# Optimization experiments

Hardware: AMD Instinct MI355X
Metric: run time of the kernel (lower is better)

## Reference

```python
import jax, jax.numpy as jnp
import numpy as np

B, C, H, N = 4, 128, 4, 2048
D = C // H  # head_dim = 32
BN_EPS = 1e-5


def _conv1(w, b, x):
    # 1x1 Conv1d: [O,C] x [B,C,N] -> [B,O,N]
    return jnp.einsum('oc,bcn->bon', w, x) + b[None, :, None]


def setup_inputs() -> dict:
    key = jax.random.key(0)
    ks = jax.random.split(key, 20)
    p = lambda k, shape: jax.random.normal(k, shape, dtype=jnp.float32) * 0.05
    return {
        'x1': jax.random.normal(ks[0], (B, C, N), dtype=jnp.float32),
        'x2': jax.random.normal(ks[1], (B, C, N), dtype=jnp.float32),
        'kv_mask': jnp.ones((B, N), dtype=bool),
        'wq': p(ks[2], (C, C)), 'bq': p(ks[3], (C,)),
        'wk': p(ks[4], (C, C)), 'bk': p(ks[5], (C,)),
        'wv': p(ks[6], (C, C)), 'bv': p(ks[7], (C,)),
        'wm': p(ks[8], (C, C)), 'bm': p(ks[9], (C,)),
        'wc1': p(ks[10], (2 * C, 2 * C)), 'bc1': p(ks[11], (2 * C,)),
        'bn_gamma': jnp.ones((2 * C,), dtype=jnp.float32),
        'bn_beta': jnp.zeros((2 * C,), dtype=jnp.float32),
        'bn_mean': p(ks[12], (2 * C,)),
        'bn_var': jax.random.uniform(ks[13], (2 * C,), dtype=jnp.float32, minval=0.5, maxval=1.5),
        'wc2': p(ks[14], (C, 2 * C)), 'bc2': p(ks[15], (C,)),
    }


def reference(x1, x2, kv_mask, wq, bq, wk, bk, wv, bv, wm, bm,
              wc1, bc1, bn_gamma, bn_beta, bn_mean, bn_var, wc2, bc2):
    b, _, n = x1.shape
    q = _conv1(wq, bq, x1).reshape(b, H, D, n)   # bhdn
    k = _conv1(wk, bk, x2).reshape(b, H, D, -1)  # bhdm
    v = _conv1(wv, bv, x2).reshape(b, H, D, -1)  # bhdm
    qk = jnp.einsum('bhdn,bhdm->bhnm', q, k)
    # masked_fill on raw QK before scaling, matching torch code
    qk = jnp.where(kv_mask[:, None, None, :], qk, jnp.float32(-1e6))
    score = jax.nn.softmax(qk * (1.0 / D ** 0.5), axis=-1)
    add_value = jnp.einsum('bhnm,bhdm->bhdn', score, v).reshape(b, C, n)
    add_value = _conv1(wm, bm, add_value)
    cat = jnp.concatenate([x1, add_value], axis=1)  # [B, 2C, N]
    h = _conv1(wc1, bc1, cat)
    # BatchNorm1d in inference mode (running stats)
    h = (h - bn_mean[None, :, None]) * jax.lax.rsqrt(bn_var[None, :, None] + BN_EPS)
    h = h * bn_gamma[None, :, None] + bn_beta[None, :, None]
    h = jax.nn.relu(h)
    h = _conv1(wc2, bc2, h)
    return x1 + h
```

## Files before the change

### kernel.cpp

```cpp
#include <hip/hip_runtime.h>

typedef __attribute__((ext_vector_type(4))) float v4f;
typedef __attribute__((ext_vector_type(8))) _Float16 half8;
typedef __attribute__((ext_vector_type(4))) _Float16 half4;
typedef __attribute__((ext_vector_type(2))) _Float16 half2t;

constexpr float C2 = 0.17677669529663687f * 1.44269504088896341f;

__device__ __forceinline__ half4 pk4(float a, float b, float c, float d) {
  half2t lo = __builtin_bit_cast(half2t, __builtin_amdgcn_cvt_pkrtz(a, b));
  half2t hi = __builtin_bit_cast(half2t, __builtin_amdgcn_cvt_pkrtz(c, d));
  return __builtin_shufflevector(lo, hi, 0, 1, 2, 3);
}

__global__ __launch_bounds__(512) void prep(
    const float* __restrict__ wq, const float* __restrict__ wk,
    const float* __restrict__ wv, const float* __restrict__ wm,
    const float* __restrict__ wc1, const float* __restrict__ wc2,
    const unsigned char* __restrict__ mask, _Float16* __restrict__ wqkvh,
    _Float16* __restrict__ wts, float* __restrict__ maskf) {
  const int e = (blockIdx.x * 512 + threadIdx.x) * 4;
  if (e < 49152) {
    const float* src;
    int base;
    if (e < 16384) { src = wq; base = 0; }
    else if (e < 32768) { src = wk; base = 16384; }
    else { src = wv; base = 32768; }
    const float4 t = *(const float4*)(src + (e - base));
    *(half4*)(wqkvh + e) = pk4(t.x, t.y, t.z, t.w);
  } else if (e < 196608) {
    const int e2 = e - 49152;
    const float* src;
    int base, cols;
    if (e2 < 16384) { src = wm; base = 0; cols = 128; }
    else if (e2 < 81920) { src = wc1; base = 16384; cols = 256; }
    else { src = wc2; base = 81920; cols = 256; }
    const int le = e2 - base;
    const int r = le / cols, c = le % cols;
    const int kt = c >> 4, q4 = (c >> 2) & 3;
    const int dst = r * cols + ((kt >> 1) << 5) + (q4 << 3) + ((kt & 1) << 2);
    const float4 t = *(const float4*)(src + le);
    *(half4*)(wts + base + dst) = pk4(t.x, t.y, t.z, t.w);
  } else {
    const int e2 = e - 196608;
    const unsigned mv = *(const unsigned*)(mask + e2);
    float4 o;
    o.x = (mv & 0x000000ffu) ? 0.f : -1.0e6f * C2;
    o.y = (mv & 0x0000ff00u) ? 0.f : -1.0e6f * C2;
    o.z = (mv & 0x00ff0000u) ? 0.f : -1.0e6f * C2;
    o.w = (mv & 0xff000000u) ? 0.f : -1.0e6f * C2;
    *(float4*)(maskf + e2) = o;
  }
}

__global__ __launch_bounds__(512, 4) void qkv(
    const float* __restrict__ x1, const float* __restrict__ x2,
    const _Float16* __restrict__ wqkvh, const float* __restrict__ bq,
    const float* __restrict__ bk, const float* __restrict__ bv,
    _Float16* __restrict__ Qpk, _Float16* __restrict__ Kpk,
    _Float16* __restrict__ Vpk) {
  const int b = blockIdx.y;
  const int bx = blockIdx.x;
  const int tid = threadIdx.x, w = tid >> 6, lane = tid & 63;
  const int l = lane & 15, q = lane >> 4;
  const int n0 = bx * 32;
  const _Float16* wqh = wqkvh;
  const _Float16* wkh = wqkvh + 16384;
  const _Float16* wvh = wqkvh + 32768;

  __shared__ _Float16 x1s[2][16 * 136];
  __shared__ _Float16 x2s[2][16 * 136];

  {
    const int ch = tid >> 2, seg = tid & 3;
#pragma unroll
    for (int g = 0; g < 2; ++g) {
      const float4 a =
          *(const float4*)(x1 + (size_t)(b * 128 + ch) * 2048 + n0 + g * 16 + seg * 4);
      const float4 c =
          *(const float4*)(x2 + (size_t)(b * 128 + ch) * 2048 + n0 + g * 16 + seg * 4);
      x1s[g][(seg * 4 + 0) * 136 + ch] = (_Float16)a.x;
      x1s[g][(seg * 4 + 1) * 136 + ch] = (_Float16)a.y;
      x1s[g][(seg * 4 + 2) * 136 + ch] = (_Float16)a.z;
      x1s[g][(seg * 4 + 3) * 136 + ch] = (_Float16)a.w;
      x2s[g][(seg * 4 + 0) * 136 + ch] = (_Float16)c.x;
      x2s[g][(seg * 4 + 1) * 136 + ch] = (_Float16)c.y;
      x2s[g][(seg * 4 + 2) * 136 + ch] = (_Float16)c.z;
      x2s[g][(seg * 4 + 3) * 136 + ch] = (_Float16)c.w;
    }
  }
  __syncthreads();

#pragma unroll
  for (int i = 0; i < 3; ++i) {
    const int t = w * 3 + i;
    if (t < 8) {
      const int mt = t;
      half8 wf[4];
#pragma unroll
      for (int kt = 0; kt < 4; ++kt)
        wf[kt] = *(const half8*)(wqh + (mt * 16 + l) * 128 + kt * 32 + q * 8);
      const v4f bias = *(const v4f*)(bq + mt * 16 + q * 4);
#pragma unroll
      for (int g = 0; g < 2; ++g) {
        v4f acc = bias;
#pragma unroll
        for (int kt = 0; kt < 4; ++kt) {
          const half8 xf = *(const half8*)&x1s[g][l * 136 + kt * 32 + q * 8];
          acc = __builtin_amdgcn_mfma_f32_16x16x32_f16(wf[kt], xf, acc, 0, 0, 0);
        }
        *(half4*)(Qpk + ((size_t)(b * 8 + mt) * 2048 + n0 + g * 16 + l) * 16 + q * 4) =
            pk4(acc[0] * C2, acc[1] * C2, acc[2] * C2, acc[3] * C2);
      }
    } else if (t < 16) {
      const int mt = t - 8;
      half8 wf[4];
#pragma unroll
      for (int kt = 0; kt < 4; ++kt)
        wf[kt] = *(const half8*)(wkh + (mt * 16 + l) * 128 + kt * 32 + q * 8);
      const v4f bias = *(const v4f*)(bk + mt * 16 + q * 4);
#pragma unroll
      for (int g = 0; g < 2; ++g) {
        v4f acc = bias;
#pragma unroll
        for (int kt = 0; kt < 4; ++kt) {
          const half8 xf = *(const half8*)&x2s[g][l * 136 + kt * 32 + q * 8];
          acc = __builtin_amdgcn_mfma_f32_16x16x32_f16(wf[kt], xf, acc, 0, 0, 0);
        }
        *(half4*)(Kpk + ((size_t)(b * 8 + mt) * 2048 + n0 + g * 16 + l) * 16 + q * 4) =
            pk4(acc[0], acc[1], acc[2], acc[3]);
      }
    } else {
      const int ot = t - 16;
      half8 wf[4];
#pragma unroll
      for (int kt = 0; kt < 4; ++kt)
        wf[kt] = *(const half8*)(wvh + (ot * 16 + l) * 128 + kt * 32 + q * 8);
      const float bvv = bv[ot * 16 + l];
#pragma unroll
      for (int g = 0; g < 2; ++g) {
        v4f acc = {bvv, bvv, bvv, bvv};
#pragma unroll
        for (int kt = 0; kt < 4; ++kt) {
          const half8 xf = *(const half8*)&x2s[g][l * 136 + kt * 32 + q * 8];
          acc = __builtin_amdgcn_mfma_f32_16x16x32_f16(xf, wf[kt], acc, 0, 0, 0);
        }
        const int kx = bx * 2 + g;
        *(half4*)(Vpk + (((size_t)(b * 4 + (ot >> 1)) * 128 + kx) * 32 +
                         (ot & 1) * 16 + l) * 16 + q * 4) =
            pk4(acc[0], acc[1], acc[2], acc[3]);
      }
    }
  }
}

__global__ __launch_bounds__(256) void attn(
    const _Float16* __restrict__ Qpk, const _Float16* __restrict__ Kpk,
    const _Float16* __restrict__ Vpk, const float* __restrict__ maskf,
    _Float16* __restrict__ Opk, float* __restrict__ lsump) {
  const int bh = blockIdx.y, b = bh >> 2, h = bh & 3;
  const int part = blockIdx.z;
  const int tid = threadIdx.x, w = tid >> 6, lane = tid & 63;
  const int l = lane & 15, q = lane >> 4;
  const int nb = blockIdx.x * 128 + w * 32;

  __shared__ _Float16 ldsK[2][3088];
  __shared__ _Float16 ldsV[2][3072];
  __shared__ __align__(16) float biass[512];

  const size_t qrow = (size_t)(b * 8 + h * 2 + (q >> 1)) * 2048;
  const half8 qf0 = *(const half8*)(Qpk + (qrow + nb + l) * 16 + (q & 1) * 8);
  const half8 qf1 = *(const half8*)(Qpk + (qrow + nb + 16 + l) * 16 + (q & 1) * 8);
  const _Float16* __restrict__ Kg = Kpk + (size_t)(b * 8 + h * 2) * 2048 * 16;
  const _Float16* __restrict__ Vg = Vpk + (size_t)((b * 4 + h) * 128) * 512;

  const int kct = tid >> 7, kk = (tid >> 1) & 63, khf = tid & 1;
  const int vt = tid >> 6, vd = (tid >> 1) & 31;

  v4f oacc[2][2] = {{{0.f, 0.f, 0.f, 0.f}, {0.f, 0.f, 0.f, 0.f}},
                    {{0.f, 0.f, 0.f, 0.f}, {0.f, 0.f, 0.f, 0.f}}};
  float ls0 = 0.f, ls1 = 0.f;
  const int mbeg = part * 512;

  if (tid < 128)
    *(float4*)&biass[tid * 4] = *(const float4*)(maskf + b * 2048 + mbeg + tid * 4);
  half8 kr = *(const half8*)(Kg + ((size_t)kct * 2048 + mbeg + kk) * 16 + khf * 8);
  half8 vr = *(const half8*)(Vg + (size_t)((mbeg >> 4) + vt) * 512 + vd * 16 + khf * 8);
  *(half8*)&ldsK[0][kct * 1544 + kk * 24 + khf * 8] = kr;
  *(half8*)&ldsV[0][vt * 768 + vd * 24 + khf * 8] = vr;
  __syncthreads();

  for (int i = 0; i < 8; ++i) {
    const int m0 = mbeg + i * 64;
    const int cur = i & 1;
    if (i < 7) {
      kr = *(const half8*)(Kg + ((size_t)kct * 2048 + m0 + 64 + kk) * 16 + khf * 8);
      vr = *(const half8*)(Vg + (size_t)(((m0 + 64) >> 4) + vt) * 512 + vd * 16 + khf * 8);
    }
    half4 pB[2][4];
#pragma unroll
    for (int mt = 0; mt < 4; ++mt) {
      const half8 kf =
          *(const half8*)&ldsK[cur][(q >> 1) * 1544 + (mt * 16 + l) * 24 + (q & 1) * 8];
      const v4f biasv = *(const v4f*)&biass[i * 64 + mt * 16 + q * 4];
      __builtin_amdgcn_s_setprio(1);
      const v4f s0 = __builtin_amdgcn_mfma_f32_16x16x32_f16(kf, qf0, biasv, 0, 0, 0);
      const v4f s1 = __builtin_amdgcn_mfma_f32_16x16x32_f16(kf, qf1, biasv, 0, 0, 0);
      __builtin_amdgcn_s_setprio(0);
      const float a0 = exp2f(s0[0]), a1 = exp2f(s0[1]), a2 = exp2f(s0[2]),
                  a3 = exp2f(s0[3]);
      const float c0 = exp2f(s1[0]), c1 = exp2f(s1[1]), c2 = exp2f(s1[2]),
                  c3 = exp2f(s1[3]);
      ls0 += (a0 + a1) + (a2 + a3);
      ls1 += (c0 + c1) + (c2 + c3);
      pB[0][mt] = pk4(a0, a1, a2, a3);
      pB[1][mt] = pk4(c0, c1, c2, c3);
    }
    __builtin_amdgcn_s_setprio(1);
#pragma unroll
    for (int mt = 0; mt < 4; ++mt) {
      const half4 vf0 = *(const half4*)&ldsV[cur][mt * 768 + l * 24 + q * 4];
      const half4 vf1 = *(const half4*)&ldsV[cur][mt * 768 + (16 + l) * 24 + q * 4];
      oacc[0][0] = __builtin_amdgcn_mfma_f32_16x16x16f16(vf0, pB[0][mt], oacc[0][0], 0, 0, 0);
      oacc[0][1] = __builtin_amdgcn_mfma_f32_16x16x16f16(vf1, pB[0][mt], oacc[0][1], 0, 0, 0);
      oacc[1][0] = __builtin_amdgcn_mfma_f32_16x16x16f16(vf0, pB[1][mt], oacc[1][0], 0, 0, 0);
      oacc[1][1] = __builtin_amdgcn_mfma_f32_16x16x16f16(vf1, pB[1][mt], oacc[1][1], 0, 0, 0);
    }
    __builtin_amdgcn_s_setprio(0);
    if (i < 7) {
      *(half8*)&ldsK[cur ^ 1][kct * 1544 + kk * 24 + khf * 8] = kr;
      *(half8*)&ldsV[cur ^ 1][vt * 768 + vd * 24 + khf * 8] = vr;
      __syncthreads();
    }
  }
  ls0 += __shfl_xor(ls0, 16);
  ls0 += __shfl_xor(ls0, 32);
  ls1 += __shfl_xor(ls1, 16);
  ls1 += __shfl_xor(ls1, 32);
  if (q == 0) {
    lsump[part * 32768 + bh * 2048 + nb + l] = ls0;
    lsump[part * 32768 + bh * 2048 + nb + 16 + l] = ls1;
  }
#pragma unroll
  for (int qt = 0; qt < 2; ++qt)
#pragma unroll
    for (int df = 0; df < 2; ++df)
      *(half4*)(Opk + (size_t)part * 1048576 +
                ((size_t)(b * 8 + h * 2 + df) * 2048 + nb + qt * 16 + l) * 16 +
                q * 4) = pk4(oacc[qt][df][0], oacc[qt][df][1], oacc[qt][df][2],
                             oacc[qt][df][3]);
}

__global__ __launch_bounds__(512, 4) void post(
    const float* __restrict__ x1, const _Float16* __restrict__ Opk,
    const float* __restrict__ lsump, const _Float16* __restrict__ wts,
    const float* __restrict__ bm, const float* __restrict__ bc1,
    const float* __restrict__ gamma, const float* __restrict__ beta,
    const float* __restrict__ mean, const float* __restrict__ var,
    const float* __restrict__ bc2, float* __restrict__ out) {
  const int b = blockIdx.y;
  const int n0 = blockIdx.x * 32;
  const int tid = threadIdx.x, w = tid >> 6, lane = tid & 63;
  const int l = lane & 15, q = lane >> 4;
  const _Float16* wm_h = wts;
  const _Float16* wc1_h = wts + 16384;
  const _Float16* wc2_h = wts + 81920;

  __shared__ __align__(16) float x1s[2][16 * 132];
  __shared__ __align__(16) _Float16 ofs[2][8 * 256];
  __shared__ __align__(16) _Float16 catl[2][16 * 256];
  __shared__ __align__(16) _Float16 exB[2][16 * 256];

  {
    const int ch = tid >> 2, seg = tid & 3;
#pragma unroll
    for (int g = 0; g < 2; ++g) {
      const float4 a =
          *(const float4*)(x1 + (size_t)(b * 128 + ch) * 2048 + n0 + g * 16 + seg * 4);
      x1s[g][(seg * 4 + 0) * 132 + ch] = a.x;
      x1s[g][(seg * 4 + 1) * 132 + ch] = a.y;
      x1s[g][(seg * 4 + 2) * 132 + ch] = a.z;
      x1s[g][(seg * 4 + 3) * 132 + ch] = a.w;
    }
  }
  {
#pragma unroll
    for (int g = 0; g < 2; ++g) {
      const int n = n0 + g * 16 + l;
      const size_t idx = (size_t)(b * 4 + (w >> 1)) * 2048 + n;
      const float rl = 1.0f / (lsump[idx] + lsump[32768 + idx] +
                               lsump[65536 + idx] + lsump[98304 + idx]);
      const size_t oa = ((size_t)(b * 8 + w) * 2048 + n) * 16 + q * 4;
      const half4 a = *(const half4*)(Opk + oa);
      const half4 c = *(const half4*)(Opk + 1048576 + oa);
      const half4 d = *(const half4*)(Opk + 2097152 + oa);
      const half4 e = *(const half4*)(Opk + 3145728 + oa);
      const _Float16 rh = (_Float16)rl;
      const half4 rl4 = {rh, rh, rh, rh};
      *(half4*)&ofs[g][w * 256 + l * 16 + q * 4] = ((a + c) + (d + e)) * rl4;
    }
  }
  __syncthreads();
  {
#pragma unroll
    for (int g = 0; g < 2; ++g) {
      const float4 xv = *(const float4*)&x1s[g][l * 132 + w * 16 + q * 4];
      *(half4*)&catl[g][w * 256 + l * 16 + q * 4] = pk4(xv.x, xv.y, xv.z, xv.w);
    }
  }
  {
    const v4f bias = *(const v4f*)(bm + w * 16 + q * 4);
    v4f acc[2] = {bias, bias};
#pragma unroll
    for (int kt2 = 0; kt2 < 4; ++kt2) {
      const half8 wp = *(const half8*)(wm_h + (w * 16 + l) * 128 + kt2 * 32 + q * 8);
      const half4 wlo = __builtin_shufflevector(wp, wp, 0, 1, 2, 3);
      const half4 whi = __builtin_shufflevector(wp, wp, 4, 5, 6, 7);
#pragma unroll
      for (int g = 0; g < 2; ++g) {
        const half4 of0 = *(const half4*)&ofs[g][(kt2 * 2) * 256 + l * 16 + q * 4];
        const half4 of1 = *(const half4*)&ofs[g][(kt2 * 2 + 1) * 256 + l * 16 + q * 4];
        acc[g] = __builtin_amdgcn_mfma_f32_16x16x16f16(wlo, of0, acc[g], 0, 0, 0);
        acc[g] = __builtin_amdgcn_mfma_f32_16x16x16f16(whi, of1, acc[g], 0, 0, 0);
      }
    }
#pragma unroll
    for (int g = 0; g < 2; ++g)
      *(half4*)&catl[g][(8 + w) * 256 + l * 16 + q * 4] =
          pk4(acc[g][0], acc[g][1], acc[g][2], acc[g][3]);
  }
  __syncthreads();
#pragma unroll
  for (int i = 0; i < 2; ++i) {
    const int mt = w * 2 + i;
    const v4f bias = *(const v4f*)(bc1 + mt * 16 + q * 4);
    v4f acc[2] = {bias, bias};
#pragma unroll
    for (int kt2 = 0; kt2 < 8; ++kt2) {
      const half8 wp = *(const half8*)(wc1_h + (mt * 16 + l) * 256 + kt2 * 32 + q * 8);
      const half4 wlo = __builtin_shufflevector(wp, wp, 0, 1, 2, 3);
      const half4 whi = __builtin_shufflevector(wp, wp, 4, 5, 6, 7);
#pragma unroll
      for (int g = 0; g < 2; ++g) {
        const half4 f0 = *(const half4*)&catl[g][(kt2 * 2) * 256 + l * 16 + q * 4];
        const half4 f1 = *(const half4*)&catl[g][(kt2 * 2 + 1) * 256 + l * 16 + q * 4];
        acc[g] = __builtin_amdgcn_mfma_f32_16x16x16f16(wlo, f0, acc[g], 0, 0, 0);
        acc[g] = __builtin_amdgcn_mfma_f32_16x16x16f16(whi, f1, acc[g], 0, 0, 0);
      }
    }
    const v4f gm = *(const v4f*)(gamma + mt * 16 + q * 4);
    const v4f bt = *(const v4f*)(beta + mt * 16 + q * 4);
    const v4f mn = *(const v4f*)(mean + mt * 16 + q * 4);
    const v4f vr = *(const v4f*)(var + mt * 16 + q * 4);
#pragma unroll
    for (int g = 0; g < 2; ++g) {
      float hh[4];
#pragma unroll
      for (int r = 0; r < 4; ++r) {
        const float a1 = gm[r] * rsqrtf(vr[r] + 1e-5f);
        const float b1 = bt[r] - mn[r] * a1;
        hh[r] = fmaxf(acc[g][r] * a1 + b1, 0.f);
      }
      *(half4*)&exB[g][mt * 256 + l * 16 + q * 4] = pk4(hh[0], hh[1], hh[2], hh[3]);
    }
  }
  __syncthreads();
  {
    const v4f bias = *(const v4f*)(bc2 + w * 16 + q * 4);
    v4f acc[2] = {bias, bias};
#pragma unroll
    for (int kt2 = 0; kt2 < 8; ++kt2) {
      const half8 wp = *(const half8*)(wc2_h + (w * 16 + l) * 256 + kt2 * 32 + q * 8);
      const half4 wlo = __builtin_shufflevector(wp, wp, 0, 1, 2, 3);
      const half4 whi = __builtin_shufflevector(wp, wp, 4, 5, 6, 7);
#pragma unroll
      for (int g = 0; g < 2; ++g) {
        const half4 f0 = *(const half4*)&exB[g][(kt2 * 2) * 256 + l * 16 + q * 4];
        const half4 f1 = *(const half4*)&exB[g][(kt2 * 2 + 1) * 256 + l * 16 + q * 4];
        acc[g] = __builtin_amdgcn_mfma_f32_16x16x16f16(wlo, f0, acc[g], 0, 0, 0);
        acc[g] = __builtin_amdgcn_mfma_f32_16x16x16f16(whi, f1, acc[g], 0, 0, 0);
      }
    }
#pragma unroll
    for (int g = 0; g < 2; ++g) {
      const int n = n0 + g * 16 + l;
#pragma unroll
      for (int r = 0; r < 4; ++r)
        out[(size_t)(b * 128 + w * 16 + q * 4 + r) * 2048 + n] =
            acc[g][r] + x1s[g][l * 132 + w * 16 + q * 4 + r];
    }
  }
}

extern "C" void kernel_launch(void* const* d_in, const int* in_sizes, int n_in,
                              void* d_out, int out_size, void* d_ws,
                              size_t ws_size, hipStream_t stream) {
  const float* x1 = (const float*)d_in[0];
  const float* x2 = (const float*)d_in[1];
  const unsigned char* kv_mask = (const unsigned char*)d_in[2];
  const float* wq = (const float*)d_in[3];
  const float* bq = (const float*)d_in[4];
  const float* wk = (const float*)d_in[5];
  const float* bk = (const float*)d_in[6];
  const float* wv = (const float*)d_in[7];
  const float* bv = (const float*)d_in[8];
  const float* wm = (const float*)d_in[9];
  const float* bm = (const float*)d_in[10];
  const float* wc1 = (const float*)d_in[11];
  const float* bc1 = (const float*)d_in[12];
  const float* bn_gamma = (const float*)d_in[13];
  const float* bn_beta = (const float*)d_in[14];
  const float* bn_mean = (const float*)d_in[15];
  const float* bn_var = (const float*)d_in[16];
  const float* wc2 = (const float*)d_in[17];
  const float* bc2 = (const float*)d_in[18];
  float* out = (float*)d_out;

  char* p = (char*)d_ws;
  _Float16* Qpk = (_Float16*)p;
  _Float16* Kpk = (_Float16*)(p + (size_t)2 * 1024 * 1024);
  _Float16* Vpk = (_Float16*)(p + (size_t)4 * 1024 * 1024);
  _Float16* Opk = (_Float16*)(p + (size_t)6 * 1024 * 1024);
  _Float16* wts = (_Float16*)(p + (size_t)14 * 1024 * 1024);
  float* lsump = (float*)(p + (size_t)14 * 1024 * 1024 + 512 * 1024);
  float* maskf = (float*)(p + (size_t)15 * 1024 * 1024);
  _Float16* wqkvh = (_Float16*)(p + (size_t)15 * 1024 * 1024 + 64 * 1024);

  prep<<<dim3(100), 512, 0, stream>>>(wq, wk, wv, wm, wc1, wc2, kv_mask,
                                      wqkvh, wts, maskf);
  qkv<<<dim3(64, 4), 512, 0, stream>>>(x1, x2, wqkvh, bq, bk, bv, Qpk, Kpk,
                                       Vpk);
  attn<<<dim3(16, 16, 4), 256, 0, stream>>>(Qpk, Kpk, Vpk, maskf, Opk, lsump);
  post<<<dim3(64, 4), 512, 0, stream>>>(x1, Opk, lsump, wts, bm, bc1,
                                        bn_gamma, bn_beta, bn_mean, bn_var,
                                        bc2, out);
}
```

Baseline: 139.3 us.

## Use 16x16x32 MFMA for PV and MLP convs with permuted K layout

Result: slower. 145.3 us (+4.3%).

```diff
diff --git a/kernel.cpp b/kernel.cpp
--- a/kernel.cpp
+++ b/kernel.cpp
@@ -11,6 +11,9 @@
   half2t lo = __builtin_bit_cast(half2t, __builtin_amdgcn_cvt_pkrtz(a, b));
   half2t hi = __builtin_bit_cast(half2t, __builtin_amdgcn_cvt_pkrtz(c, d));
   return __builtin_shufflevector(lo, hi, 0, 1, 2, 3);
+}
+__device__ __forceinline__ half8 cat8(const half4 a, const half4 b) {
+  return __builtin_shufflevector(a, b, 0, 1, 2, 3, 4, 5, 6, 7);
 }
 
 __global__ __launch_bounds__(512) void prep(
@@ -175,6 +178,8 @@
   const _Float16* __restrict__ Vg = Vpk + (size_t)((b * 4 + h) * 128) * 512;
 
   const int kct = tid >> 7, kk = (tid >> 1) & 63, khf = tid & 1;
+  const int krow = ((kk >> 5) * 2 + ((kk >> 2) & 1)) * 16 +
+                   ((kk >> 3) & 3) * 4 + (kk & 3);
   const int vt = tid >> 6, vd = (tid >> 1) & 31;
 
   v4f oacc[2][2] = {{{0.f, 0.f, 0.f, 0.f}, {0.f, 0.f, 0.f, 0.f}},
@@ -186,7 +191,7 @@
     *(float4*)&biass[tid * 4] = *(const float4*)(maskf + b * 2048 + mbeg + tid * 4);
   half8 kr = *(const half8*)(Kg + ((size_t)kct * 2048 + mbeg + kk) * 16 + khf * 8);
   half8 vr = *(const half8*)(Vg + (size_t)((mbeg >> 4) + vt) * 512 + vd * 16 + khf * 8);
-  *(half8*)&ldsK[0][kct * 1544 + kk * 24 + khf * 8] = kr;
+  *(half8*)&ldsK[0][kct * 1544 + krow * 24 + khf * 8] = kr;
   *(half8*)&ldsV[0][vt * 768 + vd * 24 + khf * 8] = vr;
   __syncthreads();
 
@@ -202,7 +207,8 @@
     for (int mt = 0; mt < 4; ++mt) {
       const half8 kf =
           *(const half8*)&ldsK[cur][(q >> 1) * 1544 + (mt * 16 + l) * 24 + (q & 1) * 8];
-      const v4f biasv = *(const v4f*)&biass[i * 64 + mt * 16 + q * 4];
+      const v4f biasv =
+          *(const v4f*)&biass[i * 64 + (mt >> 1) * 32 + q * 8 + (mt & 1) * 4];
       __builtin_amdgcn_s_setprio(1);
       const v4f s0 = __builtin_amdgcn_mfma_f32_16x16x32_f16(kf, qf0, biasv, 0, 0, 0);
       const v4f s1 = __builtin_amdgcn_mfma_f32_16x16x32_f16(kf, qf1, biasv, 0, 0, 0);
@@ -218,17 +224,22 @@
     }
     __builtin_amdgcn_s_setprio(1);
 #pragma unroll
-    for (int mt = 0; mt < 4; ++mt) {
-      const half4 vf0 = *(const half4*)&ldsV[cur][mt * 768 + l * 24 + q * 4];
-      const half4 vf1 = *(const half4*)&ldsV[cur][mt * 768 + (16 + l) * 24 + q * 4];
-      oacc[0][0] = __builtin_amdgcn_mfma_f32_16x16x16f16(vf0, pB[0][mt], oacc[0][0], 0, 0, 0);
-      oacc[0][1] = __builtin_amdgcn_mfma_f32_16x16x16f16(vf1, pB[0][mt], oacc[0][1], 0, 0, 0);
-      oacc[1][0] = __builtin_amdgcn_mfma_f32_16x16x16f16(vf0, pB[1][mt], oacc[1][0], 0, 0, 0);
-      oacc[1][1] = __builtin_amdgcn_mfma_f32_16x16x16f16(vf1, pB[1][mt], oacc[1][1], 0, 0, 0);
+    for (int mt2 = 0; mt2 < 2; ++mt2) {
+      const int vtile = mt2 * 2 + (q >> 1);
+      const half8 vf0 =
+          *(const half8*)&ldsV[cur][vtile * 768 + l * 24 + (q & 1) * 8];
+      const half8 vf1 =
+          *(const half8*)&ldsV[cur][vtile * 768 + (16 + l) * 24 + (q & 1) * 8];
+      const half8 p0 = cat8(pB[0][mt2 * 2], pB[0][mt2 * 2 + 1]);
+      const half8 p1 = cat8(pB[1][mt2 * 2], pB[1][mt2 * 2 + 1]);
+      oacc[0][0] = __builtin_amdgcn_mfma_f32_16x16x32_f16(vf0, p0, oacc[0][0], 0, 0, 0);
+      oacc[0][1] = __builtin_amdgcn_mfma_f32_16x16x32_f16(vf1, p0, oacc[0][1], 0, 0, 0);
+      oacc[1][0] = __builtin_amdgcn_mfma_f32_16x16x32_f16(vf0, p1, oacc[1][0], 0, 0, 0);
+      oacc[1][1] = __builtin_amdgcn_mfma_f32_16x16x32_f16(vf1, p1, oacc[1][1], 0, 0, 0);
     }
     __builtin_amdgcn_s_setprio(0);
     if (i < 7) {
-      *(half8*)&ldsK[cur ^ 1][kct * 1544 + kk * 24 + khf * 8] = kr;
+      *(half8*)&ldsK[cur ^ 1][kct * 1544 + krow * 24 + khf * 8] = kr;
       *(half8*)&ldsV[cur ^ 1][vt * 768 + vd * 24 + khf * 8] = vr;
       __syncthreads();
     }
@@ -314,14 +325,11 @@
 #pragma unroll
     for (int kt2 = 0; kt2 < 4; ++kt2) {
       const half8 wp = *(const half8*)(wm_h + (w * 16 + l) * 128 + kt2 * 32 + q * 8);
-      const half4 wlo = __builtin_shufflevector(wp, wp, 0, 1, 2, 3);
-      const half4 whi = __builtin_shufflevector(wp, wp, 4, 5, 6, 7);
 #pragma unroll
       for (int g = 0; g < 2; ++g) {
         const half4 of0 = *(const half4*)&ofs[g][(kt2 * 2) * 256 + l * 16 + q * 4];
         const half4 of1 = *(const half4*)&ofs[g][(kt2 * 2 + 1) * 256 + l * 16 + q * 4];
-        acc[g] = __builtin_amdgcn_mfma_f32_16x16x16f16(wlo, of0, acc[g], 0, 0, 0);
-        acc[g] = __builtin_amdgcn_mfma_f32_16x16x16f16(whi, of1, acc[g], 0, 0, 0);
+        acc[g] = __builtin_amdgcn_mfma_f32_16x16x32_f16(wp, cat8(of0, of1), acc[g], 0, 0, 0);
       }
     }
 #pragma unroll
@@ -338,14 +346,11 @@
 #pragma unroll
     for (int kt2 = 0; kt2 < 8; ++kt2) {
       const half8 wp = *(const half8*)(wc1_h + (mt * 16 + l) * 256 + kt2 * 32 + q * 8);
-      const half4 wlo = __builtin_shufflevector(wp, wp, 0, 1, 2, 3);
-      const half4 whi = __builtin_shufflevector(wp, wp, 4, 5, 6, 7);
 #pragma unroll
       for (int g = 0; g < 2; ++g) {
         const half4 f0 = *(const half4*)&catl[g][(kt2 * 2) * 256 + l * 16 + q * 4];
         const half4 f1 = *(const half4*)&catl[g][(kt2 * 2 + 1) * 256 + l * 16 + q * 4];
-        acc[g] = __builtin_amdgcn_mfma_f32_16x16x16f16(wlo, f0, acc[g], 0, 0, 0);
-        acc[g] = __builtin_amdgcn_mfma_f32_16x16x16f16(whi, f1, acc[g], 0, 0, 0);
+        acc[g] = __builtin_amdgcn_mfma_f32_16x16x32_f16(wp, cat8(f0, f1), acc[g], 0, 0, 0);
       }
     }
     const v4f gm = *(const v4f*)(gamma + mt * 16 + q * 4);
@@ -371,14 +376,11 @@
 #pragma unroll
     for (int kt2 = 0; kt2 < 8; ++kt2) {
       const half8 wp = *(const half8*)(wc2_h + (w * 16 + l) * 256 + kt2 * 32 + q * 8);
-      const half4 wlo = __builtin_shufflevector(wp, wp, 0, 1, 2, 3);
-      const half4 whi = __builtin_shufflevector(wp, wp, 4, 5, 6, 7);
 #pragma unroll
       for (int g = 0; g < 2; ++g) {
         const half4 f0 = *(const half4*)&exB[g][(kt2 * 2) * 256 + l * 16 + q * 4];
         const half4 f1 = *(const half4*)&exB[g][(kt2 * 2 + 1) * 256 + l * 16 + q * 4];
-        acc[g] = __builtin_amdgcn_mfma_f32_16x16x16f16(wlo, f0, acc[g], 0, 0, 0);
-        acc[g] = __builtin_amdgcn_mfma_f32_16x16x16f16(whi, f1, acc[g], 0, 0, 0);
+        acc[g] = __builtin_amdgcn_mfma_f32_16x16x32_f16(wp, cat8(f0, f1), acc[g], 0, 0, 0);
       }
     }
 #pragma unroll
```
